# Kernel optimization log

Hardware: AMD Instinct MI355X
Metric: run time of the kernel (lower is better)

Reference implementation:

```python
import jax, jax.numpy as jnp
import numpy as np

N = 50000        # nodes
E = 800000       # edges
H = 128          # in = hidden = out width
L = 4            # num_layers
BN_EPS = 1e-5


def _bn(x, g, b):
    # training-mode batch norm over the node dimension (biased variance, as torch)
    mu = jnp.mean(x, axis=0)
    var = jnp.mean((x - mu) ** 2, axis=0)
    return (x - mu) * jax.lax.rsqrt(var + BN_EPS) * g + b


def setup_inputs() -> dict:
    key = jax.random.key(0)
    ks = jax.random.split(key, 16)
    s = 0.05
    return {
        "x": jax.random.normal(ks[0], (N, H), dtype=jnp.float32),
        "edge_index": jax.random.randint(ks[1], (2, E), 0, N, dtype=jnp.int32),
        # stacked per-layer MLP params (all layers share dims H->H->H)
        "fc1_w": jax.random.normal(ks[2], (L, H, H), dtype=jnp.float32) * s,
        "fc1_b": jnp.zeros((L, H), dtype=jnp.float32),
        "bn1_g": jnp.ones((L, H), dtype=jnp.float32),
        "bn1_b": jnp.zeros((L, H), dtype=jnp.float32),
        "fc2_w": jax.random.normal(ks[3], (L, H, H), dtype=jnp.float32) * s,
        "fc2_b": jnp.zeros((L, H), dtype=jnp.float32),
        "bn2_g": jnp.ones((L, H), dtype=jnp.float32),
        "bn2_b": jnp.zeros((L, H), dtype=jnp.float32),
        # outer per-layer BatchNorm (intended one-per-GIN-layer)
        "bn3_g": jnp.ones((L, H), dtype=jnp.float32),
        "bn3_b": jnp.zeros((L, H), dtype=jnp.float32),
        # final classifier
        "fc_w": jax.random.normal(ks[4], (H, H), dtype=jnp.float32) * s,
        "fc_b": jnp.zeros((H,), dtype=jnp.float32),
    }


def reference(x, edge_index, fc1_w, fc1_b, bn1_g, bn1_b, fc2_w, fc2_b,
              bn2_g, bn2_b, bn3_g, bn3_b, fc_w, fc_b):
    src = edge_index[0]
    dst = edge_index[1]
    for i in range(L):
        # GINConv, eps=0: h = MLP((1+eps)*x + sum_{j in N(v)} x_j)
        agg = jax.ops.segment_sum(x[src], dst, num_segments=N)  # [N, H]
        h = x + agg
        # MLP: relu(bn1(fc1(h))) -> bn2(fc2(.))
        h = jax.nn.relu(_bn(h @ fc1_w[i].T + fc1_b[i], bn1_g[i], bn1_b[i]))
        h = _bn(h @ fc2_w[i].T + fc2_b[i], bn2_g[i], bn2_b[i])
        # outer BN + ReLU per layer
        x = jax.nn.relu(_bn(h, bn3_g[i], bn3_b[i]))
    return x @ fc_w.T + fc_b  # [N, H]
```

## Files before the change

kernel.cpp:

```cpp
#include <hip/hip_runtime.h>

#define NN 50000
#define HD 128
#define NL 4
#define BN_EPS 1e-5f
#define NTILES 3125
#define MAXDEG 64

typedef __attribute__((ext_vector_type(8))) short short8;
typedef __attribute__((ext_vector_type(4))) float f32x4;
typedef __attribute__((ext_vector_type(4))) uint uint4v;

__device__ inline ushort f2bf(float f){
  uint u = __float_as_uint(f);
  uint r = (u + 0x7fffu + ((u >> 16) & 1u)) >> 16;
  return (ushort)r;
}
__device__ inline float bflo(uint u){ return __uint_as_float(u << 16); }
__device__ inline float bfhi(uint u){ return __uint_as_float(u & 0xffff0000u); }
__device__ inline uint pk2(float lo, float hi){
  return (uint)f2bf(lo) | ((uint)f2bf(hi) << 16);
}

__global__ __launch_bounds__(256) void cast_all(const float* __restrict__ x,
                                                const float* __restrict__ w1,
                                                const float* __restrict__ w2,
                                                const float* __restrict__ wf,
                                                ushort* __restrict__ xb,
                                                ushort* __restrict__ wb,
                                                uint* __restrict__ zptr){
  const int ZB4 = 16600;
  {
    int z = blockIdx.x * 256 + threadIdx.x;
    int zstride = gridDim.x * 256;
    uint4v zero = (uint4v)0u;
    for (; z < ZB4; z += zstride) ((uint4v*)zptr)[z] = zero;
  }
  const int NX = NN * HD / 4;
  const int NT = NX + 36864;
  int i = blockIdx.x * 256 + threadIdx.x;
  int stride = gridDim.x * 256;
  for (; i < NT; i += stride){
    const float* src; ushort* dst;
    if (i < NX){ src = x + i * 4; dst = xb + i * 4; }
    else {
      int k = i - NX;
      dst = wb + k * 4;
      if (k < 16384)      src = w1 + k * 4;
      else if (k < 32768) src = w2 + (k - 16384) * 4;
      else                src = wf + (k - 32768) * 4;
    }
    float4 v = *(const float4*)src;
    ushort4 r;
    r.x = f2bf(v.x); r.y = f2bf(v.y); r.z = f2bf(v.z); r.w = f2bf(v.w);
    *(ushort4*)dst = r;
  }
}

__global__ void fill1_kernel(const int* __restrict__ dst, int* __restrict__ cnt,
                             int* __restrict__ pos, int E){
  int e = (blockIdx.x * 256 + threadIdx.x) * 4;
  if (e + 4 <= E){
    int4 d = *(const int4*)(dst + e);
    int4 p;
    p.x = atomicAdd(&cnt[d.x], 1);
    p.y = atomicAdd(&cnt[d.y], 1);
    p.z = atomicAdd(&cnt[d.z], 1);
    p.w = atomicAdd(&cnt[d.w], 1);
    *(int4*)(pos + e) = p;
  } else {
    for (; e < E; ++e) pos[e] = atomicAdd(&cnt[dst[e]], 1);
  }
}

__global__ void fill2_kernel(const int* __restrict__ src, const int* __restrict__ dst,
                             const int* __restrict__ pos, int* __restrict__ slots, int E){
  int e = (blockIdx.x * 256 + threadIdx.x) * 4;
  if (e + 4 <= E){
    int4 d = *(const int4*)(dst + e);
    int4 p = *(const int4*)(pos + e);
    int4 s = *(const int4*)(src + e);
    slots[d.x * MAXDEG + p.x] = s.x;
    slots[d.y * MAXDEG + p.y] = s.y;
    slots[d.z * MAXDEG + p.z] = s.z;
    slots[d.w * MAXDEG + p.w] = s.w;
  } else {
    for (; e < E; ++e) slots[dst[e] * MAXDEG + pos[e]] = src[e];
  }
}

__device__ inline void bn_params8(const float* __restrict__ st, const float* __restrict__ gA,
                                  const float* __restrict__ gB, const float* __restrict__ bB,
                                  int mode, float* sS, float* sT){
  int c = threadIdx.x;
  if (c < 128){
    float s0 = 0.f, s1 = 0.f;
#pragma unroll
    for (int k = 0; k < 8; ++k){
      s0 += st[k * 256 + c];
      s1 += st[k * 256 + 128 + c];
    }
    const float invN = 1.f / (float)NN;
    float mu = s0 * invN;
    float var = fmaxf(s1 * invN - mu * mu, 0.f);
    float S, T;
    if (mode == 0){
      S = gA[c] * rsqrtf(var + BN_EPS);
      T = gB[c] - mu * S;
    } else {
      float inv2 = rsqrtf(var + BN_EPS);
      float tt = gA[c] * inv2;
      float inv3 = rsqrtf(tt * tt * var + BN_EPS);
      S = tt * inv3 * gB[c];
      T = bB[c] - mu * S;
    }
    sS[c] = S; sT[c] = T;
  }
}

template<bool AFF>
__global__ __launch_bounds__(512, 2) void aggemm_t(const ushort* __restrict__ xin,
                                                   const int* __restrict__ deg,
                                                   const int* __restrict__ slots,
                                                   const ushort* __restrict__ W,
                                                   const float* __restrict__ bias,
                                                   ushort* __restrict__ Yb,
                                                   float* __restrict__ statsOut,
                                                   const float* __restrict__ statsIn,
                                                   const float* __restrict__ g2,
                                                   const float* __restrict__ g3,
                                                   const float* __restrict__ b3){
  __shared__ uint4v w4[128 * 17];
  __shared__ uint4v a4[8][16 * 17];
  __shared__ float ssum[128];
  __shared__ float ssq[128];
  __shared__ float sS[128];
  __shared__ float sT[128];

  const uint4v* Wg = (const uint4v*)W;
  for (int c = threadIdx.x; c < 2048; c += 512){
    w4[(c >> 4) * 17 + (c & 15)] = Wg[c];
  }
  if (AFF) bn_params8(statsIn, g2, g3, b3, 1, sS, sT);
  if (threadIdx.x < 128){ ssum[threadIdx.x] = 0.f; ssq[threadIdx.x] = 0.f; }
  __syncthreads();

  int wave = threadIdx.x >> 6;
  int lane = threadIdx.x & 63;
  int grp  = lane >> 4;
  int col  = lane & 15;
  int tile = blockIdx.x * 8 + wave;
  bool tv = tile < NTILES;

  float S[8], T[8];
  if (AFF){
#pragma unroll
    for (int k = 0; k < 8; ++k){ S[k] = sS[col * 8 + k]; T[k] = sT[col * 8 + k]; }
  }

  const uint4v* x4 = (const uint4v*)xin;

#define INIT8(v)                                                                \
  if (AFF){                                                                     \
    a[0]=fmaxf(bflo((v).x)*S[0]+T[0],0.f); a[1]=fmaxf(bfhi((v).x)*S[1]+T[1],0.f); \
    a[2]=fmaxf(bflo((v).y)*S[2]+T[2],0.f); a[3]=fmaxf(bfhi((v).y)*S[3]+T[3],0.f); \
    a[4]=fmaxf(bflo((v).z)*S[4]+T[4],0.f); a[5]=fmaxf(bfhi((v).z)*S[5]+T[5],0.f); \
    a[6]=fmaxf(bflo((v).w)*S[6]+T[6],0.f); a[7]=fmaxf(bfhi((v).w)*S[7]+T[7],0.f); \
  } else {                                                                      \
    a[0]=bflo((v).x); a[1]=bfhi((v).x); a[2]=bflo((v).y); a[3]=bfhi((v).y);     \
    a[4]=bflo((v).z); a[5]=bfhi((v).z); a[6]=bflo((v).w); a[7]=bfhi((v).w);     \
  }

#define ACC8(v)                                                                 \
  if (AFF){                                                                     \
    a[0]+=fmaxf(bflo((v).x)*S[0]+T[0],0.f); a[1]+=fmaxf(bfhi((v).x)*S[1]+T[1],0.f); \
    a[2]+=fmaxf(bflo((v).y)*S[2]+T[2],0.f); a[3]+=fmaxf(bfhi((v).y)*S[3]+T[3],0.f); \
    a[4]+=fmaxf(bflo((v).z)*S[4]+T[4],0.f); a[5]+=fmaxf(bfhi((v).z)*S[5]+T[5],0.f); \
    a[6]+=fmaxf(bflo((v).w)*S[6]+T[6],0.f); a[7]+=fmaxf(bfhi((v).w)*S[7]+T[7],0.f); \
  } else {                                                                      \
    a[0]+=bflo((v).x); a[1]+=bfhi((v).x); a[2]+=bflo((v).y); a[3]+=bfhi((v).y); \
    a[4]+=bflo((v).z); a[5]+=bfhi((v).z); a[6]+=bflo((v).w); a[7]+=bfhi((v).w); \
  }

  if (tv){
    for (int it = 0; it < 4; ++it){
      int node = tile * 16 + it * 4 + grp;
      int e = deg[node];
      const int* sl = slots + node * MAXDEG;
      float a[8];
      {
        uint4v v = x4[node * 16 + col];
        INIT8(v);
      }
      int j = 0;
      for (; j + 8 <= e; j += 8){
        int i0 = sl[j+0], i1 = sl[j+1], i2 = sl[j+2], i3 = sl[j+3];
        int i4 = sl[j+4], i5 = sl[j+5], i6 = sl[j+6], i7 = sl[j+7];
        uint4v v0 = x4[i0 * 16 + col];
        uint4v v1 = x4[i1 * 16 + col];
        uint4v v2 = x4[i2 * 16 + col];
        uint4v v3 = x4[i3 * 16 + col];
        uint4v v4 = x4[i4 * 16 + col];
        uint4v v5 = x4[i5 * 16 + col];
        uint4v v6 = x4[i6 * 16 + col];
        uint4v v7 = x4[i7 * 16 + col];
        ACC8(v0); ACC8(v1); ACC8(v2); ACC8(v3);
        ACC8(v4); ACC8(v5); ACC8(v6); ACC8(v7);
      }
      for (; j + 4 <= e; j += 4){
        int i0 = sl[j+0], i1 = sl[j+1], i2 = sl[j+2], i3 = sl[j+3];
        uint4v v0 = x4[i0 * 16 + col];
        uint4v v1 = x4[i1 * 16 + col];
        uint4v v2 = x4[i2 * 16 + col];
        uint4v v3 = x4[i3 * 16 + col];
        ACC8(v0); ACC8(v1); ACC8(v2); ACC8(v3);
      }
      for (; j < e; ++j){
        uint4v v = x4[sl[j] * 16 + col];
        ACC8(v);
      }
      uint4v o;
      o.x = pk2(a[0], a[1]); o.y = pk2(a[2], a[3]);
      o.z = pk2(a[4], a[5]); o.w = pk2(a[6], a[7]);
      a4[wave][(it * 4 + grp) * 17 + col] = o;
    }
  }
#undef INIT8
#undef ACC8
  __syncthreads();

  int m = lane & 15, q = lane >> 4;
  f32x4 acc[8];
#pragma unroll
  for (int i = 0; i < 8; ++i) acc[i] = (f32x4)0.f;

#pragma unroll
  for (int kt = 0; kt < 4; ++kt){
    uint4v t = a4[wave][m * 17 + kt * 4 + q];
    short8 af = *(short8*)&t;
#pragma unroll
    for (int to = 0; to < 8; ++to){
      uint4v bw = w4[(to * 16 + m) * 17 + kt * 4 + q];
      acc[to] = __builtin_amdgcn_mfma_f32_16x16x32_bf16(af, *(short8*)&bw, acc[to], 0, 0, 0);
    }
  }

#pragma unroll
  for (int to = 0; to < 8; ++to){
    int colo = to * 16 + m;
    float bc = bias[colo];
    float ls = 0.f, lq = 0.f;
    if (tv){
#pragma unroll
      for (int r = 0; r < 4; ++r){
        float v = acc[to][r] + bc;
        int row = tile * 16 + q * 4 + r;
        __builtin_nontemporal_store(__builtin_bit_cast(ushort, f2bf(v)), Yb + row * 128 + colo);
        ls += v; lq += v * v;
      }
    }
    ls += __shfl_xor(ls, 16); lq += __shfl_xor(lq, 16);
    ls += __shfl_xor(ls, 32); lq += __shfl_xor(lq, 32);
    if (tv && q == 0){ atomicAdd(&ssum[colo], ls); atomicAdd(&ssq[colo], lq); }
  }
  __syncthreads();
  if (threadIdx.x < 128){
    int sb = (blockIdx.x & 7) * 256;
    atomicAdd(&statsOut[sb + threadIdx.x], ssum[threadIdx.x]);
    atomicAdd(&statsOut[sb + 128 + threadIdx.x], ssq[threadIdx.x]);
  }
}

__global__ __launch_bounds__(512) void gemm_kernel(const ushort* __restrict__ A,
                                                   const ushort* __restrict__ W,
                                                   const float* __restrict__ bias,
                                                   ushort* __restrict__ Yb,
                                                   float* __restrict__ Yf,
                                                   float* __restrict__ statsOut,
                                                   const float* __restrict__ statsIn,
                                                   const float* __restrict__ gA,
                                                   const float* __restrict__ gB,
                                                   const float* __restrict__ bB,
                                                   int mode){
  __shared__ uint4v w4[128 * 17];
  __shared__ float ssum[128];
  __shared__ float ssq[128];
  __shared__ float sS[128];
  __shared__ float sT[128];
  const uint4v* Wg = (const uint4v*)W;
  for (int c = threadIdx.x; c < 2048; c += 512){
    w4[(c >> 4) * 17 + (c & 15)] = Wg[c];
  }
  if (statsIn) bn_params8(statsIn, gA, gB, bB, mode, sS, sT);
  if (threadIdx.x < 128){ ssum[threadIdx.x] = 0.f; ssq[threadIdx.x] = 0.f; }
  __syncthreads();

  int wave = threadIdx.x >> 6;
  int lane = threadIdx.x & 63;
  int m = lane & 15, q = lane >> 4;
  int tile = blockIdx.x * 8 + wave;
  bool tv = tile < NTILES;
  const uint4v* A4 = (const uint4v*)A;

  f32x4 acc[8];
#pragma unroll
  for (int i = 0; i < 8; ++i) acc[i] = (f32x4)0.f;

#pragma unroll
  for (int kt = 0; kt < 4; ++kt){
    short8 af = (short8)0;
    if (tv){
      uint4v t = __builtin_nontemporal_load(A4 + (tile * 16 + m) * 16 + kt * 4 + q);
      if (statsIn){
        int kc = kt * 32 + q * 8;
        uint4v pk;
        pk.x = pk2(fmaxf(bflo(t.x)*sS[kc+0]+sT[kc+0],0.f),
                   fmaxf(bfhi(t.x)*sS[kc+1]+sT[kc+1],0.f));
        pk.y = pk2(fmaxf(bflo(t.y)*sS[kc+2]+sT[kc+2],0.f),
                   fmaxf(bfhi(t.y)*sS[kc+3]+sT[kc+3],0.f));
        pk.z = pk2(fmaxf(bflo(t.z)*sS[kc+4]+sT[kc+4],0.f),
                   fmaxf(bfhi(t.z)*sS[kc+5]+sT[kc+5],0.f));
        pk.w = pk2(fmaxf(bflo(t.w)*sS[kc+6]+sT[kc+6],0.f),
                   fmaxf(bfhi(t.w)*sS[kc+7]+sT[kc+7],0.f));
        t = pk;
      }
      af = *(short8*)&t;
    }
#pragma unroll
    for (int to = 0; to < 8; ++to){
      uint4v bw = w4[(to * 16 + m) * 17 + kt * 4 + q];
      acc[to] = __builtin_amdgcn_mfma_f32_16x16x32_bf16(af, *(short8*)&bw, acc[to], 0, 0, 0);
    }
  }

  bool dost = (statsOut != nullptr);
#pragma unroll
  for (int to = 0; to < 8; ++to){
    int col = to * 16 + m;
    float bc = bias[col];
    float ls = 0.f, lq = 0.f;
    if (tv){
#pragma unroll
      for (int r = 0; r < 4; ++r){
        float v = acc[to][r] + bc;
        int row = tile * 16 + q * 4 + r;
        if (Yb) __builtin_nontemporal_store(__builtin_bit_cast(ushort, f2bf(v)), Yb + row * 128 + col);
        else    __builtin_nontemporal_store(v, Yf + row * 128 + col);
        ls += v; lq += v * v;
      }
    }
    if (dost){
      ls += __shfl_xor(ls, 16); lq += __shfl_xor(lq, 16);
      ls += __shfl_xor(ls, 32); lq += __shfl_xor(lq, 32);
      if (tv && q == 0){ atomicAdd(&ssum[col], ls); atomicAdd(&ssq[col], lq); }
    }
  }
  if (dost){
    __syncthreads();
    if (threadIdx.x < 128){
      int sb = (blockIdx.x & 7) * 256;
      atomicAdd(&statsOut[sb + threadIdx.x], ssum[threadIdx.x]);
      atomicAdd(&statsOut[sb + 128 + threadIdx.x], ssq[threadIdx.x]);
    }
  }
}

extern "C" void kernel_launch(void* const* d_in, const int* in_sizes, int n_in,
                              void* d_out, int out_size, void* d_ws, size_t ws_size,
                              hipStream_t stream) {
  const float* x     = (const float*)d_in[0];
  const int*   ei    = (const int*)d_in[1];
  const float* fc1_w = (const float*)d_in[2];
  const float* fc1_b = (const float*)d_in[3];
  const float* bn1_g = (const float*)d_in[4];
  const float* bn1_b = (const float*)d_in[5];
  const float* fc2_w = (const float*)d_in[6];
  const float* fc2_b = (const float*)d_in[7];
  const float* bn2_g = (const float*)d_in[8];
  const float* bn3_g = (const float*)d_in[10];
  const float* bn3_b = (const float*)d_in[11];
  const float* fc_w  = (const float*)d_in[12];
  const float* fc_b  = (const float*)d_in[13];

  int E = in_sizes[1] / 2;
  const int* srcp = ei;
  const int* dstp = ei + E;

  char* ws = (char*)d_ws;
  int*    cnt    = (int*)(ws + 0);
  float*  stats  = (float*)(ws + 200064);
  int*    pos    = (int*)(ws + 265600);
  int*    slots  = (int*)(ws + 3465600);
  ushort* wb     = (ushort*)(ws + 16265600);
  ushort* xb     = (ushort*)(ws + 16560512);
  ushort* y1b    = (ushort*)(ws + 29360512);
  ushort* y2b    = (ushort*)(ws + 42160512);

  cast_all<<<2048, 256, 0, stream>>>(x, fc1_w, fc2_w, fc_w, xb, wb, (uint*)ws);

  const int EB4 = (E / 4 + 255) / 256 + 1;
  fill1_kernel<<<EB4, 256, 0, stream>>>(dstp, cnt, pos, E);
  fill2_kernel<<<EB4, 256, 0, stream>>>(srcp, dstp, pos, slots, E);

  const int gb = (NTILES + 7) / 8;

  for (int i = 0; i < NL; ++i){
    if (i == 0){
      aggemm_t<false><<<gb, 512, 0, stream>>>(xb, cnt, slots, wb + i * 16384,
                                              fc1_b + i * 128, y1b,
                                              stats + (i * 2) * 2048,
                                              nullptr, nullptr, nullptr, nullptr);
    } else {
      aggemm_t<true><<<gb, 512, 0, stream>>>(y2b, cnt, slots, wb + i * 16384,
                                             fc1_b + i * 128, y1b,
                                             stats + (i * 2) * 2048,
                                             stats + ((i - 1) * 2 + 1) * 2048,
                                             bn2_g + (i - 1) * 128,
                                             bn3_g + (i - 1) * 128,
                                             bn3_b + (i - 1) * 128);
    }
    gemm_kernel<<<gb, 512, 0, stream>>>(y1b, wb + 65536 + i * 16384, fc2_b + i * 128,
                                        y2b, nullptr, stats + (i * 2 + 1) * 2048,
                                        stats + (i * 2) * 2048, bn1_g + i * 128,
                                        bn1_b + i * 128, nullptr, 0);
  }

  gemm_kernel<<<gb, 512, 0, stream>>>(y2b, wb + 131072, fc_b,
                                      nullptr, (float*)d_out, nullptr,
                                      stats + 7 * 2048, bn2_g + 384,
                                      bn3_g + 384, bn3_b + 384, 1);
}
```

Measured before the change: 463.8 us.

## Split aggregation-GEMM tiles across wave pairs and raise occupancy with swizzled LDS

Each 16-row tile in the fused aggregate+GEMM kernel is now handled by two waves. Each wave gathers half the rows and computes half the output columns, so a block covers 4 tiles instead of 8 and the grid doubles. The weight tile in LDS drops its padding in favour of an XOR swizzle, and the per-block LDS shrinks. The launch bound asks for 6 blocks per CU instead of 2, aiming at more waves in flight to hide gather latency. The trade-off is that the weight matrix is loaded into LDS by twice as many blocks, and the register cap may cause spills.

```diff
diff --git a/kernel.cpp b/kernel.cpp
--- a/kernel.cpp
+++ b/kernel.cpp
@@ -6,6 +6,7 @@
 #define BN_EPS 1e-5f
 #define NTILES 3125
 #define MAXDEG 64
+#define WSWZ(e) ((e) ^ (((e) >> 4) & 3))
 
 typedef __attribute__((ext_vector_type(8))) short short8;
 typedef __attribute__((ext_vector_type(4))) float f32x4;
@@ -119,7 +120,7 @@
 }
 
 template<bool AFF>
-__global__ __launch_bounds__(512, 2) void aggemm_t(const ushort* __restrict__ xin,
+__global__ __launch_bounds__(512, 6) void aggemm_t(const ushort* __restrict__ xin,
                                                    const int* __restrict__ deg,
                                                    const int* __restrict__ slots,
                                                    const ushort* __restrict__ W,
@@ -130,8 +131,8 @@
                                                    const float* __restrict__ g2,
                                                    const float* __restrict__ g3,
                                                    const float* __restrict__ b3){
-  __shared__ uint4v w4[128 * 17];
-  __shared__ uint4v a4[8][16 * 17];
+  __shared__ uint4v w4[2048];
+  __shared__ uint4v a4[4][16 * 17];
   __shared__ float ssum[128];
   __shared__ float ssq[128];
   __shared__ float sS[128];
@@ -139,7 +140,7 @@
 
   const uint4v* Wg = (const uint4v*)W;
   for (int c = threadIdx.x; c < 2048; c += 512){
-    w4[(c >> 4) * 17 + (c & 15)] = Wg[c];
+    w4[WSWZ(c)] = Wg[c];
   }
   if (AFF) bn_params8(statsIn, g2, g3, b3, 1, sS, sT);
   if (threadIdx.x < 128){ ssum[threadIdx.x] = 0.f; ssq[threadIdx.x] = 0.f; }
@@ -147,9 +148,11 @@
 
   int wave = threadIdx.x >> 6;
   int lane = threadIdx.x & 63;
+  int tl   = wave >> 1;
+  int hf   = wave & 1;
   int grp  = lane >> 4;
   int col  = lane & 15;
-  int tile = blockIdx.x * 8 + wave;
+  int tile = blockIdx.x * 4 + tl;
   bool tv = tile < NTILES;
 
   float S[8], T[8];
@@ -183,8 +186,9 @@
   }
 
   if (tv){
-    for (int it = 0; it < 4; ++it){
-      int node = tile * 16 + it * 4 + grp;
+    for (int it = 0; it < 2; ++it){
+      int lrow = hf * 8 + it * 4 + grp;
+      int node = tile * 16 + lrow;
       int e = deg[node];
       const int* sl = slots + node * MAXDEG;
       float a[8];
@@ -222,7 +226,7 @@
       uint4v o;
       o.x = pk2(a[0], a[1]); o.y = pk2(a[2], a[3]);
       o.z = pk2(a[4], a[5]); o.w = pk2(a[6], a[7]);
-      a4[wave][(it * 4 + grp) * 17 + col] = o;
+      a4[tl][lrow * 17 + col] = o;
     }
   }
 #undef INIT8
@@ -230,30 +234,32 @@
   __syncthreads();
 
   int m = lane & 15, q = lane >> 4;
-  f32x4 acc[8];
-#pragma unroll
-  for (int i = 0; i < 8; ++i) acc[i] = (f32x4)0.f;
+  f32x4 acc[4];
+#pragma unroll
+  for (int i = 0; i < 4; ++i) acc[i] = (f32x4)0.f;
 
 #pragma unroll
   for (int kt = 0; kt < 4; ++kt){
-    uint4v t = a4[wave][m * 17 + kt * 4 + q];
+    uint4v t = a4[tl][m * 17 + kt * 4 + q];
     short8 af = *(short8*)&t;
 #pragma unroll
-    for (int to = 0; to < 8; ++to){
-      uint4v bw = w4[(to * 16 + m) * 17 + kt * 4 + q];
-      acc[to] = __builtin_amdgcn_mfma_f32_16x16x32_bf16(af, *(short8*)&bw, acc[to], 0, 0, 0);
-    }
-  }
-
-#pragma unroll
-  for (int to = 0; to < 8; ++to){
-    int colo = to * 16 + m;
+    for (int t4 = 0; t4 < 4; ++t4){
+      int to = hf * 4 + t4;
+      int e = (to * 16 + m) * 16 + kt * 4 + q;
+      uint4v bw = w4[WSWZ(e)];
+      acc[t4] = __builtin_amdgcn_mfma_f32_16x16x32_bf16(af, *(short8*)&bw, acc[t4], 0, 0, 0);
+    }
+  }
+
+#pragma unroll
+  for (int t4 = 0; t4 < 4; ++t4){
+    int colo = (hf * 4 + t4) * 16 + m;
     float bc = bias[colo];
     float ls = 0.f, lq = 0.f;
     if (tv){
 #pragma unroll
       for (int r = 0; r < 4; ++r){
-        float v = acc[to][r] + bc;
+        float v = acc[t4][r] + bc;
         int row = tile * 16 + q * 4 + r;
         __builtin_nontemporal_store(__builtin_bit_cast(ushort, f2bf(v)), Yb + row * 128 + colo);
         ls += v; lq += v * v;
@@ -402,16 +408,17 @@
   fill1_kernel<<<EB4, 256, 0, stream>>>(dstp, cnt, pos, E);
   fill2_kernel<<<EB4, 256, 0, stream>>>(srcp, dstp, pos, slots, E);
 
+  const int ga = (NTILES + 3) / 4;
   const int gb = (NTILES + 7) / 8;
 
   for (int i = 0; i < NL; ++i){
     if (i == 0){
-      aggemm_t<false><<<gb, 512, 0, stream>>>(xb, cnt, slots, wb + i * 16384,
+      aggemm_t<false><<<ga, 512, 0, stream>>>(xb, cnt, slots, wb + i * 16384,
                                               fc1_b + i * 128, y1b,
                                               stats + (i * 2) * 2048,
                                               nullptr, nullptr, nullptr, nullptr);
     } else {
-      aggemm_t<true><<<gb, 512, 0, stream>>>(y2b, cnt, slots, wb + i * 16384,
+      aggemm_t<true><<<ga, 512, 0, stream>>>(y2b, cnt, slots, wb + i * 16384,
                                              fc1_b + i * 128, y1b,
                                              stats + (i * 2) * 2048,
                                              stats + ((i - 1) * 2 + 1) * 2048,
```

Result: no change. 464.7 us (+0.2%).
